# Kernel optimization log

Measured on AMD Instinct MI355X. Metric: run time of the kernel, lower is better.

## Reference

```python
import jax, jax.numpy as jnp
import numpy as np

N = 12500      # nodes
E = 200000     # edges (avg degree 16)
IN = 32        # inp_dim
OUT = 32       # out_dim
ATTN = 32      # attn_rel_emb_dim
R = 200        # num_rels
NB = 50        # num_bases


def setup_inputs() -> dict:
    key = jax.random.key(0)
    ks = jax.random.split(key, 10)
    node_feat = jax.random.normal(ks[0], (N, IN), jnp.float32)
    total_edge = jax.random.randint(ks[1], (2, E), 0, N)
    total_target_relation = jax.random.normal(ks[2], (E, ATTN), jnp.float32)
    total_relation_embed = jax.random.normal(ks[3], (E, ATTN), jnp.float32)
    total_relation = jax.random.randint(ks[4], (E,), 0, R)
    # learned parameters (xavier-ish scale)
    weight = jax.random.normal(ks[5], (NB, IN, OUT), jnp.float32) * 0.1
    w_comp = jax.random.normal(ks[6], (R, NB), jnp.float32) * 0.1
    self_loop_weight = jax.random.normal(ks[7], (IN, OUT), jnp.float32) * 0.1
    A_w = jax.random.normal(ks[8], (IN, 2 * IN + 2 * ATTN), jnp.float32) * 0.1
    A_b = jnp.zeros((IN,), jnp.float32)
    B_w = jax.random.normal(ks[9], (1, IN), jnp.float32) * 0.1
    B_b = jnp.zeros((1,), jnp.float32)
    return {
        'node_feat': node_feat,
        'total_target_relation': total_target_relation,
        'total_relation_embed': total_relation_embed,
        'weight': weight,
        'w_comp': w_comp,
        'self_loop_weight': self_loop_weight,
        'A_w': A_w,
        'A_b': A_b,
        'B_w': B_w,
        'B_b': B_b,
        'total_edge': total_edge,
        'total_relation': total_relation,
    }


def reference(node_feat, total_target_relation, total_relation_embed,
              weight, w_comp, self_loop_weight, A_w, A_b, B_w, B_b,
              total_edge, total_relation):
    # basis decomposition: per-relation weight [R, IN, OUT]
    rel_w = jnp.einsum('rb,bio->rio', w_comp, weight)
    src = node_feat[total_edge[0]]            # [E, IN]
    tgt = node_feat[total_edge[1]]            # [E, IN]
    # per-edge relation-specific transform (bmm in torch)
    msg = jnp.einsum('ei,eio->eo', src, rel_w[total_relation])  # [E, OUT]
    curr = tgt @ self_loop_weight             # [E, OUT]
    # attention MLP: sigmoid(B(relu(A(concat))))
    e = jnp.concatenate([src, tgt, total_relation_embed, total_target_relation], axis=1)
    h = jax.nn.relu(e @ A_w.T + A_b)
    a = jax.nn.sigmoid(h @ B_w.T + B_b)       # [E, 1]
    curr = curr + msg * a
    # gnn_spmm(e2n_sp, curr): scatter-add edge messages to target nodes
    out = jax.ops.segment_sum(curr, total_edge[1], num_segments=node_feat.shape[0])
    return out  # [N, OUT]
```

## Files before the change

### kernel.cpp

```cpp
#include <hip/hip_runtime.h>

#define N_NODES 12500
#define N_EDGES 200000
#define DIM 32
#define N_REL 200
#define N_BASES 50

#define OUT_ELEMS   (N_NODES * DIM)
#define ZERO_BLOCKS ((OUT_ELEMS + 1023) / 1024)

#define EDGES_PER_HBLOCK 1024
#define HIST_BLOCKS ((N_EDGES + EDGES_PER_HBLOCK - 1) / EDGES_PER_HBLOCK)

#define AWBF_OFF  409600
#define SLWT_OFF  417792
#define BINS_OFF  419840
#define GCUR_OFF  420640
#define PERM_OFF  421440
#define WS_A (PERM_OFF + N_EDGES * 16)
#define WS_B (PERM_OFF + N_EDGES * 4)

typedef __attribute__((ext_vector_type(8))) short short8;
typedef __attribute__((ext_vector_type(4))) float f32x4;
typedef __attribute__((ext_vector_type(4))) unsigned short us4;

__device__ __forceinline__ unsigned short f2bf(float x) {
    union { float f; unsigned u; } v; v.f = x;
    unsigned r = (v.u + 0x7FFFu + ((v.u >> 16) & 1u)) >> 16;
    return (unsigned short)r;
}
__device__ __forceinline__ float bf2f(unsigned short u) {
    return __uint_as_float(((unsigned)u) << 16);
}

__device__ __forceinline__ short8 cvt8(float4 a, float4 b) {
    short8 r;
    r[0] = (short)f2bf(a.x); r[1] = (short)f2bf(a.y);
    r[2] = (short)f2bf(a.z); r[3] = (short)f2bf(a.w);
    r[4] = (short)f2bf(b.x); r[5] = (short)f2bf(b.y);
    r[6] = (short)f2bf(b.z); r[7] = (short)f2bf(b.w);
    return r;
}

__device__ __forceinline__ int clampi(int x, int hi) {
    return x < 0 ? 0 : (x >= hi ? hi - 1 : x);
}

#define MFMA(A, B, C) __builtin_amdgcn_mfma_f32_16x16x32_bf16(A, B, C, 0, 0, 0)

__global__ __launch_bounds__(256) void prep_kernel(
    const float* __restrict__ weight,
    const float* __restrict__ w_comp,
    const float* __restrict__ Aw,
    const float* __restrict__ slw,
    const int*  __restrict__ rel,
    unsigned short* __restrict__ relw_bf,
    unsigned short* __restrict__ aw_bf,
    unsigned short* __restrict__ slwT_bf,
    int* __restrict__ bins,
    float* __restrict__ out,
    int sorted)
{
    int b = blockIdx.x, tid = threadIdx.x;
    if (b < N_REL) {
        __shared__ float wc[N_BASES];
        if (tid < N_BASES) wc[tid] = w_comp[b * N_BASES + tid];
        __syncthreads();
        const float* wp = weight + tid * 4;
        float4 acc = make_float4(0.f, 0.f, 0.f, 0.f);
        #pragma unroll 10
        for (int bb = 0; bb < N_BASES; bb++) {
            float4 w = *(const float4*)(wp + bb * 1024);
            float c = wc[bb];
            acc.x = fmaf(c, w.x, acc.x); acc.y = fmaf(c, w.y, acc.y);
            acc.z = fmaf(c, w.z, acc.z); acc.w = fmaf(c, w.w, acc.w);
        }
        int i = (tid * 4) >> 5, o = (tid * 4) & 31;
        if (sorted) {
            relw_bf[b * 1024 + (o + 0) * 32 + i] = f2bf(acc.x);
            relw_bf[b * 1024 + (o + 1) * 32 + i] = f2bf(acc.y);
            relw_bf[b * 1024 + (o + 2) * 32 + i] = f2bf(acc.z);
            relw_bf[b * 1024 + (o + 3) * 32 + i] = f2bf(acc.w);
        } else {
            us4 ov;
            ov[0] = f2bf(acc.x); ov[1] = f2bf(acc.y);
            ov[2] = f2bf(acc.z); ov[3] = f2bf(acc.w);
            *(us4*)(relw_bf + b * 1024 + tid * 4) = ov;
        }
    } else if (b < N_REL + ZERO_BLOCKS) {
        int base = (b - N_REL) * 1024 + tid * 4;
        if (base + 3 < OUT_ELEMS)
            *(float4*)(out + base) = make_float4(0.f, 0.f, 0.f, 0.f);
        else
            for (int k = 0; k < 4; k++)
                if (base + k < OUT_ELEMS) out[base + k] = 0.f;
    } else if (b == N_REL + ZERO_BLOCKS) {
        for (int x = tid; x < 32 * 128; x += 256) aw_bf[x] = f2bf(Aw[x]);
        for (int x = tid; x < 32 * 32; x += 256) {
            int i = x >> 5, j = x & 31;
            slwT_bf[j * 32 + i] = f2bf(slw[x]);
        }
    } else {
        __shared__ int lb[N_REL];
        if (tid < N_REL) lb[tid] = 0;
        __syncthreads();
        int base = (b - (N_REL + ZERO_BLOCKS + 1)) * EDGES_PER_HBLOCK + tid;
        #pragma unroll
        for (int k = 0; k < 4; k++) {
            int e = base + k * 256;
            if (e < N_EDGES) atomicAdd(&lb[clampi(rel[e], N_REL)], 1);
        }
        __syncthreads();
        if (tid < N_REL && lb[tid] > 0) atomicAdd(&bins[tid], lb[tid]);
    }
}

__global__ __launch_bounds__(256) void scatter_kernel(
    const int* __restrict__ rel,
    const int* __restrict__ edge0,
    const int* __restrict__ edge1,
    const int* __restrict__ bins,
    int* __restrict__ gcur,
    int4* __restrict__ perm4,
    int* __restrict__ permi)
{
    __shared__ int sb[N_REL];
    __shared__ int pref[N_REL];
    __shared__ int lb[N_REL];
    int tid = threadIdx.x;
    if (tid < N_REL) { sb[tid] = bins[tid]; lb[tid] = 0; }
    __syncthreads();
    if (tid == 0) {
        int run = 0;
        for (int r = 0; r < N_REL; r++) { pref[r] = run; run += sb[r]; }
    }
    __syncthreads();
    int base = blockIdx.x * EDGES_PER_HBLOCK + tid;
    int myr[4], myrank[4];
    #pragma unroll
    for (int k = 0; k < 4; k++) {
        int e = base + k * 256;
        myr[k] = -1;
        if (e < N_EDGES) {
            myr[k] = clampi(rel[e], N_REL);
            myrank[k] = atomicAdd(&lb[myr[k]], 1);
        }
    }
    __syncthreads();
    if (tid < N_REL) {
        int c = lb[tid];
        lb[tid] = c > 0 ? (pref[tid] + atomicAdd(&gcur[tid], c)) : 0;
    }
    __syncthreads();
    #pragma unroll
    for (int k = 0; k < 4; k++) {
        if (myr[k] >= 0) {
            int e = base + k * 256;
            int pos = lb[myr[k]] + myrank[k];
            if (perm4) {
                int s = clampi(edge0[e], N_NODES);
                int t = clampi(edge1[e], N_NODES);
                perm4[pos] = make_int4(s, t, myr[k], e);
            } else {
                permi[pos] = e;
            }
        }
    }
}

__global__ __launch_bounds__(256) void edge_kernel(
    const float* __restrict__ node_feat,
    const float* __restrict__ ttr,
    const float* __restrict__ tre,
    const float* __restrict__ Ab,
    const float* __restrict__ Bw,
    const float* __restrict__ Bb,
    const int*  __restrict__ edge0,
    const int*  __restrict__ edge1,
    const int*  __restrict__ rel,
    const int4* __restrict__ perm4,
    const int*  __restrict__ permi,
    const unsigned short* __restrict__ relw_bf,
    const unsigned short* __restrict__ aw_bf,
    const unsigned short* __restrict__ slwT_bf,
    float* __restrict__ out)
{
    __shared__ float msgL[4 * 16 * 36];

    int tid  = threadIdx.x;
    int wave = tid >> 6;
    int lane = tid & 63;
    int m = lane & 15;
    int q = lane >> 4;
    int base = blockIdx.x * 64 + wave * 16;

    int s_ld = 0, t_ld = 0, r_ld = 0, e_ld = 0;
    if (lane < 16) {
        if (perm4) {
            int4 pv = perm4[base + lane];
            s_ld = pv.x; t_ld = pv.y; r_ld = pv.z; e_ld = pv.w;
        } else {
            int eid = permi ? clampi(permi[base + lane], N_EDGES) : (base + lane);
            e_ld = eid;
            s_ld = clampi(edge0[eid], N_NODES);
            t_ld = clampi(edge1[eid], N_NODES);
            r_ld = clampi(rel[eid],   N_REL);
        }
    }
    int s_m   = __shfl(s_ld, m, 64);
    int t_m   = __shfl(t_ld, m, 64);
    int eid_m = __shfl(e_ld, m, 64);
    int r_m   = __shfl(r_ld, m, 64);
    int r0    = __shfl(r_ld, 0, 64);
    bool sorted = (perm4 != nullptr) || (permi != nullptr);

    const float* sp = node_feat + s_m * DIM + q * 8;
    float4 sv0 = *(const float4*)sp, sv1 = *(const float4*)(sp + 4);
    const float* tp = node_feat + t_m * DIM + q * 8;
    float4 tv0 = *(const float4*)tp, tv1 = *(const float4*)(tp + 4);
    const float* rp = tre + eid_m * DIM + q * 8;
    float4 rv0 = *(const float4*)rp, rv1 = *(const float4*)(rp + 4);
    const float* qp = ttr + eid_m * DIM + q * 8;
    float4 qv0 = *(const float4*)qp, qv1 = *(const float4*)(qp + 4);

    short8 fsrc = cvt8(sv0, sv1);
    short8 ftgt = cvt8(tv0, tv1);
    short8 fre  = cvt8(rv0, rv1);
    short8 ftr  = cvt8(qv0, qv1);

    short8 bA[4][2], bS[2];
    #pragma unroll
    for (int hh = 0; hh < 2; hh++) {
        #pragma unroll
        for (int c = 0; c < 4; c++)
            bA[c][hh] = *(const short8*)(aw_bf + (16 * hh + m) * 128 + 32 * c + 8 * q);
        bS[hh] = *(const short8*)(slwT_bf + (16 * hh + m) * 32 + 8 * q);
    }

    float ab0 = Ab[m], ab1 = Ab[16 + m];
    f32x4 hacc0 = {ab0, ab0, ab0, ab0};
    f32x4 hacc1 = {ab1, ab1, ab1, ab1};
    f32x4 cacc0 = {0.f, 0.f, 0.f, 0.f};
    f32x4 cacc1 = {0.f, 0.f, 0.f, 0.f};

    hacc0 = MFMA(fsrc, bA[0][0], hacc0);  hacc1 = MFMA(fsrc, bA[0][1], hacc1);
    hacc0 = MFMA(ftgt, bA[1][0], hacc0);  hacc1 = MFMA(ftgt, bA[1][1], hacc1);
    hacc0 = MFMA(fre,  bA[2][0], hacc0);  hacc1 = MFMA(fre,  bA[2][1], hacc1);
    hacc0 = MFMA(ftr,  bA[3][0], hacc0);  hacc1 = MFMA(ftr,  bA[3][1], hacc1);
    cacc0 = MFMA(ftgt, bS[0], cacc0);     cacc1 = MFMA(ftgt, bS[1], cacc1);

    f32x4 macc0 = {0.f, 0.f, 0.f, 0.f};
    f32x4 macc1 = {0.f, 0.f, 0.f, 0.f};
    bool uni = sorted && __all(r_m == r0);
    if (uni) {
        const unsigned short* rwt = relw_bf + r0 * 1024;
        short8 bM0 = *(const short8*)(rwt + m * 32 + 8 * q);
        short8 bM1 = *(const short8*)(rwt + (16 + m) * 32 + 8 * q);
        macc0 = MFMA(fsrc, bM0, macc0);
        macc1 = MFMA(fsrc, bM1, macc1);
    } else {
        int e_loc = lane >> 2;
        int cq    = lane & 3;
        int r_e = __shfl(r_ld, e_loc, 64);
        float sf[8] = {sv0.x, sv0.y, sv0.z, sv0.w, sv1.x, sv1.y, sv1.z, sv1.w};
        float msg[8] = {0.f, 0.f, 0.f, 0.f, 0.f, 0.f, 0.f, 0.f};
        const unsigned short* rw = relw_bf + r_e * 1024;
        #pragma unroll 4
        for (int k = 0; k < 32; k++) {
            float s_k = __shfl(sf[k & 7], e_loc + 16 * (k >> 3), 64);
            if (sorted) {
                #pragma unroll
                for (int p = 0; p < 8; p++)
                    msg[p] = fmaf(s_k, bf2f(rw[(cq * 8 + p) * 32 + k]), msg[p]);
            } else {
                union { short8 s; unsigned u[4]; } W;
                W.s = *(const short8*)(rw + k * 32 + cq * 8);
                #pragma unroll
                for (int p = 0; p < 4; p++) {
                    msg[2 * p]     = fmaf(s_k, __uint_as_float(W.u[p] << 16), msg[2 * p]);
                    msg[2 * p + 1] = fmaf(s_k, __uint_as_float(W.u[p] & 0xffff0000u), msg[2 * p + 1]);
                }
            }
        }
        float* ml = msgL + wave * (16 * 36);
        *(float4*)(ml + e_loc * 36 + cq * 8)     = make_float4(msg[0], msg[1], msg[2], msg[3]);
        *(float4*)(ml + e_loc * 36 + cq * 8 + 4) = make_float4(msg[4], msg[5], msg[6], msg[7]);
        #pragma unroll
        for (int v = 0; v < 4; v++) {
            macc0[v] = ml[(4 * q + v) * 36 + m];
            macc1[v] = ml[(4 * q + v) * 36 + 16 + m];
        }
    }

    float bw0 = Bw[m], bw1 = Bw[16 + m], Bb0 = Bb[0];
    float av[4];
    #pragma unroll
    for (int v = 0; v < 4; v++) {
        float p = fmaxf(hacc0[v], 0.f) * bw0 + fmaxf(hacc1[v], 0.f) * bw1;
        p += __shfl_xor(p, 1, 16);
        p += __shfl_xor(p, 2, 16);
        p += __shfl_xor(p, 4, 16);
        p += __shfl_xor(p, 8, 16);
        av[v] = 1.f / (1.f + __expf(-(p + Bb0)));
    }
    #pragma unroll
    for (int v = 0; v < 4; v++) {
        int row = 4 * q + v;
        int tv = __shfl(t_ld, row, 64);
        atomicAdd(&out[tv * DIM + m],      cacc0[v] + macc0[v] * av[v]);
        atomicAdd(&out[tv * DIM + 16 + m], cacc1[v] + macc1[v] * av[v]);
    }
}

extern "C" void kernel_launch(void* const* d_in, const int* in_sizes, int n_in,
                              void* d_out, int out_size, void* d_ws, size_t ws_size,
                              hipStream_t stream) {
    const float* node_feat = (const float*)d_in[0];
    const float* ttr       = (const float*)d_in[1];
    const float* tre       = (const float*)d_in[2];
    const float* weight    = (const float*)d_in[3];
    const float* w_comp    = (const float*)d_in[4];
    const float* slw       = (const float*)d_in[5];
    const float* Aw        = (const float*)d_in[6];
    const float* Ab        = (const float*)d_in[7];
    const float* Bw        = (const float*)d_in[8];
    const float* Bb        = (const float*)d_in[9];
    const int*  total_edge = (const int*)d_in[10];
    const int*  rel        = (const int*)d_in[11];
    const int*  edge0 = total_edge;
    const int*  edge1 = total_edge + N_EDGES;

    unsigned short* relw_bf = (unsigned short*)d_ws;
    unsigned short* aw_bf   = (unsigned short*)((char*)d_ws + AWBF_OFF);
    unsigned short* slwT_bf = (unsigned short*)((char*)d_ws + SLWT_OFF);
    int* bins = (int*)((char*)d_ws + BINS_OFF);
    int* gcur = (int*)((char*)d_ws + GCUR_OFF);
    float* out = (float*)d_out;

    int tierA = ws_size >= (size_t)WS_A;
    int tierB = !tierA && ws_size >= (size_t)WS_B;
    int sorted = tierA || tierB;
    int4* perm4 = tierA ? (int4*)((char*)d_ws + PERM_OFF) : nullptr;
    int*  permi = tierB ? (int*)((char*)d_ws + PERM_OFF) : nullptr;

    if (sorted) hipMemsetAsync(bins, 0, 1600, stream);

    int prep_blocks = N_REL + ZERO_BLOCKS + 1 + (sorted ? HIST_BLOCKS : 0);
    prep_kernel<<<prep_blocks, 256, 0, stream>>>(
        weight, w_comp, Aw, slw, rel, relw_bf, aw_bf, slwT_bf, bins, out, sorted);

    if (sorted)
        scatter_kernel<<<HIST_BLOCKS, 256, 0, stream>>>(
            rel, edge0, edge1, bins, gcur, perm4, permi);

    edge_kernel<<<N_EDGES / 64, 256, 0, stream>>>(
        node_feat, ttr, tre, Ab, Bw, Bb,
        edge0, edge1, rel, perm4, permi,
        relw_bf, aw_bf, slwT_bf, out);
}
```

Baseline: 159.5 us.

## Process 64 edges per wave in four sub-batches to amortize weight loads

Each wave now handles 64 edges instead of 16. It loads all 64 edge indices with one coalesced per-lane load and reuses the attention and self-loop weight fragments across four 16-edge MFMA sub-batches. It also checks whether the whole 64-edge wave shares one relation, so the relation weight is loaded once; otherwise it checks each 16-edge sub-batch. The grid shrinks fourfold, which cuts per-block setup and repeated weight fetches but lowers the number of resident waves available to hide gather latency. It may also raise register pressure from the unrolled loop.

```diff
diff --git a/kernel.cpp b/kernel.cpp
--- a/kernel.cpp
+++ b/kernel.cpp
@@ -192,41 +192,22 @@
     int lane = tid & 63;
     int m = lane & 15;
     int q = lane >> 4;
-    int base = blockIdx.x * 64 + wave * 16;
-
-    int s_ld = 0, t_ld = 0, r_ld = 0, e_ld = 0;
-    if (lane < 16) {
-        if (perm4) {
-            int4 pv = perm4[base + lane];
-            s_ld = pv.x; t_ld = pv.y; r_ld = pv.z; e_ld = pv.w;
-        } else {
-            int eid = permi ? clampi(permi[base + lane], N_EDGES) : (base + lane);
-            e_ld = eid;
-            s_ld = clampi(edge0[eid], N_NODES);
-            t_ld = clampi(edge1[eid], N_NODES);
-            r_ld = clampi(rel[eid],   N_REL);
-        }
-    }
-    int s_m   = __shfl(s_ld, m, 64);
-    int t_m   = __shfl(t_ld, m, 64);
-    int eid_m = __shfl(e_ld, m, 64);
-    int r_m   = __shfl(r_ld, m, 64);
-    int r0    = __shfl(r_ld, 0, 64);
+    int base = blockIdx.x * 256 + wave * 64;
+    if (base >= N_EDGES) return;
+
     bool sorted = (perm4 != nullptr) || (permi != nullptr);
 
-    const float* sp = node_feat + s_m * DIM + q * 8;
-    float4 sv0 = *(const float4*)sp, sv1 = *(const float4*)(sp + 4);
-    const float* tp = node_feat + t_m * DIM + q * 8;
-    float4 tv0 = *(const float4*)tp, tv1 = *(const float4*)(tp + 4);
-    const float* rp = tre + eid_m * DIM + q * 8;
-    float4 rv0 = *(const float4*)rp, rv1 = *(const float4*)(rp + 4);
-    const float* qp = ttr + eid_m * DIM + q * 8;
-    float4 qv0 = *(const float4*)qp, qv1 = *(const float4*)(qp + 4);
-
-    short8 fsrc = cvt8(sv0, sv1);
-    short8 ftgt = cvt8(tv0, tv1);
-    short8 fre  = cvt8(rv0, rv1);
-    short8 ftr  = cvt8(qv0, qv1);
+    int s_l, t_l, r_l, e_l;
+    if (perm4) {
+        int4 pv = perm4[base + lane];
+        s_l = pv.x; t_l = pv.y; r_l = pv.z; e_l = pv.w;
+    } else {
+        int eid = permi ? clampi(permi[base + lane], N_EDGES) : (base + lane);
+        e_l = eid;
+        s_l = clampi(edge0[eid], N_NODES);
+        t_l = clampi(edge1[eid], N_NODES);
+        r_l = clampi(rel[eid],   N_REL);
+    }
 
     short8 bA[4][2], bS[2];
     #pragma unroll
@@ -236,79 +217,115 @@
             bA[c][hh] = *(const short8*)(aw_bf + (16 * hh + m) * 128 + 32 * c + 8 * q);
         bS[hh] = *(const short8*)(slwT_bf + (16 * hh + m) * 32 + 8 * q);
     }
-
     float ab0 = Ab[m], ab1 = Ab[16 + m];
-    f32x4 hacc0 = {ab0, ab0, ab0, ab0};
-    f32x4 hacc1 = {ab1, ab1, ab1, ab1};
-    f32x4 cacc0 = {0.f, 0.f, 0.f, 0.f};
-    f32x4 cacc1 = {0.f, 0.f, 0.f, 0.f};
-
-    hacc0 = MFMA(fsrc, bA[0][0], hacc0);  hacc1 = MFMA(fsrc, bA[0][1], hacc1);
-    hacc0 = MFMA(ftgt, bA[1][0], hacc0);  hacc1 = MFMA(ftgt, bA[1][1], hacc1);
-    hacc0 = MFMA(fre,  bA[2][0], hacc0);  hacc1 = MFMA(fre,  bA[2][1], hacc1);
-    hacc0 = MFMA(ftr,  bA[3][0], hacc0);  hacc1 = MFMA(ftr,  bA[3][1], hacc1);
-    cacc0 = MFMA(ftgt, bS[0], cacc0);     cacc1 = MFMA(ftgt, bS[1], cacc1);
-
-    f32x4 macc0 = {0.f, 0.f, 0.f, 0.f};
-    f32x4 macc1 = {0.f, 0.f, 0.f, 0.f};
-    bool uni = sorted && __all(r_m == r0);
-    if (uni) {
+    float bw0 = Bw[m], bw1 = Bw[16 + m], Bb0 = Bb[0];
+
+    int r0 = __shfl(r_l, 0, 64);
+    bool uniWave = sorted && __all(r_l == r0);
+    short8 bM0w = {}, bM1w = {};
+    if (uniWave) {
         const unsigned short* rwt = relw_bf + r0 * 1024;
-        short8 bM0 = *(const short8*)(rwt + m * 32 + 8 * q);
-        short8 bM1 = *(const short8*)(rwt + (16 + m) * 32 + 8 * q);
-        macc0 = MFMA(fsrc, bM0, macc0);
-        macc1 = MFMA(fsrc, bM1, macc1);
-    } else {
-        int e_loc = lane >> 2;
-        int cq    = lane & 3;
-        int r_e = __shfl(r_ld, e_loc, 64);
-        float sf[8] = {sv0.x, sv0.y, sv0.z, sv0.w, sv1.x, sv1.y, sv1.z, sv1.w};
-        float msg[8] = {0.f, 0.f, 0.f, 0.f, 0.f, 0.f, 0.f, 0.f};
-        const unsigned short* rw = relw_bf + r_e * 1024;
-        #pragma unroll 4
-        for (int k = 0; k < 32; k++) {
-            float s_k = __shfl(sf[k & 7], e_loc + 16 * (k >> 3), 64);
-            if (sorted) {
-                #pragma unroll
-                for (int p = 0; p < 8; p++)
-                    msg[p] = fmaf(s_k, bf2f(rw[(cq * 8 + p) * 32 + k]), msg[p]);
-            } else {
-                union { short8 s; unsigned u[4]; } W;
-                W.s = *(const short8*)(rw + k * 32 + cq * 8);
-                #pragma unroll
-                for (int p = 0; p < 4; p++) {
-                    msg[2 * p]     = fmaf(s_k, __uint_as_float(W.u[p] << 16), msg[2 * p]);
-                    msg[2 * p + 1] = fmaf(s_k, __uint_as_float(W.u[p] & 0xffff0000u), msg[2 * p + 1]);
+        bM0w = *(const short8*)(rwt + m * 32 + 8 * q);
+        bM1w = *(const short8*)(rwt + (16 + m) * 32 + 8 * q);
+    }
+
+    #pragma unroll
+    for (int sb = 0; sb < 4; sb++) {
+        int lb = sb * 16;
+        int s_m   = __shfl(s_l, lb + m, 64);
+        int t_m   = __shfl(t_l, lb + m, 64);
+        int eid_m = __shfl(e_l, lb + m, 64);
+
+        const float* sp = node_feat + s_m * DIM + q * 8;
+        float4 sv0 = *(const float4*)sp, sv1 = *(const float4*)(sp + 4);
+        const float* tp = node_feat + t_m * DIM + q * 8;
+        float4 tv0 = *(const float4*)tp, tv1 = *(const float4*)(tp + 4);
+        const float* rp = tre + eid_m * DIM + q * 8;
+        float4 rv0 = *(const float4*)rp, rv1 = *(const float4*)(rp + 4);
+        const float* qp = ttr + eid_m * DIM + q * 8;
+        float4 qv0 = *(const float4*)qp, qv1 = *(const float4*)(qp + 4);
+
+        short8 fsrc = cvt8(sv0, sv1);
+        short8 ftgt = cvt8(tv0, tv1);
+        short8 fre  = cvt8(rv0, rv1);
+        short8 ftr  = cvt8(qv0, qv1);
+
+        f32x4 hacc0 = {ab0, ab0, ab0, ab0};
+        f32x4 hacc1 = {ab1, ab1, ab1, ab1};
+        f32x4 cacc0 = {0.f, 0.f, 0.f, 0.f};
+        f32x4 cacc1 = {0.f, 0.f, 0.f, 0.f};
+
+        hacc0 = MFMA(fsrc, bA[0][0], hacc0);  hacc1 = MFMA(fsrc, bA[0][1], hacc1);
+        hacc0 = MFMA(ftgt, bA[1][0], hacc0);  hacc1 = MFMA(ftgt, bA[1][1], hacc1);
+        hacc0 = MFMA(fre,  bA[2][0], hacc0);  hacc1 = MFMA(fre,  bA[2][1], hacc1);
+        hacc0 = MFMA(ftr,  bA[3][0], hacc0);  hacc1 = MFMA(ftr,  bA[3][1], hacc1);
+        cacc0 = MFMA(ftgt, bS[0], cacc0);     cacc1 = MFMA(ftgt, bS[1], cacc1);
+
+        f32x4 macc0 = {0.f, 0.f, 0.f, 0.f};
+        f32x4 macc1 = {0.f, 0.f, 0.f, 0.f};
+        int r_sb = __shfl(r_l, lb + m, 64);
+        int r00  = __shfl(r_l, lb, 64);
+        bool uni = uniWave || (sorted && __all(r_sb == r00));
+        if (uni) {
+            short8 bM0 = bM0w, bM1 = bM1w;
+            if (!uniWave) {
+                const unsigned short* rwt = relw_bf + r00 * 1024;
+                bM0 = *(const short8*)(rwt + m * 32 + 8 * q);
+                bM1 = *(const short8*)(rwt + (16 + m) * 32 + 8 * q);
+            }
+            macc0 = MFMA(fsrc, bM0, macc0);
+            macc1 = MFMA(fsrc, bM1, macc1);
+        } else {
+            int e_loc = lane >> 2;
+            int cq    = lane & 3;
+            int r_e = __shfl(r_l, lb + e_loc, 64);
+            float sf[8] = {sv0.x, sv0.y, sv0.z, sv0.w, sv1.x, sv1.y, sv1.z, sv1.w};
+            float msg[8] = {0.f, 0.f, 0.f, 0.f, 0.f, 0.f, 0.f, 0.f};
+            const unsigned short* rw = relw_bf + r_e * 1024;
+            #pragma unroll 4
+            for (int k = 0; k < 32; k++) {
+                float s_k = __shfl(sf[k & 7], e_loc + 16 * (k >> 3), 64);
+                if (sorted) {
+                    #pragma unroll
+                    for (int p = 0; p < 8; p++)
+                        msg[p] = fmaf(s_k, bf2f(rw[(cq * 8 + p) * 32 + k]), msg[p]);
+                } else {
+                    union { short8 s; unsigned u[4]; } W;
+                    W.s = *(const short8*)(rw + k * 32 + cq * 8);
+                    #pragma unroll
+                    for (int p = 0; p < 4; p++) {
+                        msg[2 * p]     = fmaf(s_k, __uint_as_float(W.u[p] << 16), msg[2 * p]);
+                        msg[2 * p + 1] = fmaf(s_k, __uint_as_float(W.u[p] & 0xffff0000u), msg[2 * p + 1]);
+                    }
                 }
             }
-        }
-        float* ml = msgL + wave * (16 * 36);
-        *(float4*)(ml + e_loc * 36 + cq * 8)     = make_float4(msg[0], msg[1], msg[2], msg[3]);
-        *(float4*)(ml + e_loc * 36 + cq * 8 + 4) = make_float4(msg[4], msg[5], msg[6], msg[7]);
+            float* ml = msgL + wave * (16 * 36);
+            *(float4*)(ml + e_loc * 36 + cq * 8)     = make_float4(msg[0], msg[1], msg[2], msg[3]);
+            *(float4*)(ml + e_loc * 36 + cq * 8 + 4) = make_float4(msg[4], msg[5], msg[6], msg[7]);
+            #pragma unroll
+            for (int v = 0; v < 4; v++) {
+                macc0[v] = ml[(4 * q + v) * 36 + m];
+                macc1[v] = ml[(4 * q + v) * 36 + 16 + m];
+            }
+        }
+
+        float av[4];
         #pragma unroll
         for (int v = 0; v < 4; v++) {
-            macc0[v] = ml[(4 * q + v) * 36 + m];
-            macc1[v] = ml[(4 * q + v) * 36 + 16 + m];
-        }
-    }
-
-    float bw0 = Bw[m], bw1 = Bw[16 + m], Bb0 = Bb[0];
-    float av[4];
-    #pragma unroll
-    for (int v = 0; v < 4; v++) {
-        float p = fmaxf(hacc0[v], 0.f) * bw0 + fmaxf(hacc1[v], 0.f) * bw1;
-        p += __shfl_xor(p, 1, 16);
-        p += __shfl_xor(p, 2, 16);
-        p += __shfl_xor(p, 4, 16);
-        p += __shfl_xor(p, 8, 16);
-        av[v] = 1.f / (1.f + __expf(-(p + Bb0)));
-    }
-    #pragma unroll
-    for (int v = 0; v < 4; v++) {
-        int row = 4 * q + v;
-        int tv = __shfl(t_ld, row, 64);
-        atomicAdd(&out[tv * DIM + m],      cacc0[v] + macc0[v] * av[v]);
-        atomicAdd(&out[tv * DIM + 16 + m], cacc1[v] + macc1[v] * av[v]);
+            float p = fmaxf(hacc0[v], 0.f) * bw0 + fmaxf(hacc1[v], 0.f) * bw1;
+            p += __shfl_xor(p, 1, 16);
+            p += __shfl_xor(p, 2, 16);
+            p += __shfl_xor(p, 4, 16);
+            p += __shfl_xor(p, 8, 16);
+            av[v] = 1.f / (1.f + __expf(-(p + Bb0)));
+        }
+        #pragma unroll
+        for (int v = 0; v < 4; v++) {
+            int row = 4 * q + v;
+            int tv = __shfl(t_l, lb + row, 64);
+            atomicAdd(&out[tv * DIM + m],      cacc0[v] + macc0[v] * av[v]);
+            atomicAdd(&out[tv * DIM + 16 + m], cacc1[v] + macc1[v] * av[v]);
+        }
     }
 }
 
@@ -353,7 +370,7 @@
         scatter_kernel<<<HIST_BLOCKS, 256, 0, stream>>>(
             rel, edge0, edge1, bins, gcur, perm4, permi);
 
-    edge_kernel<<<N_EDGES / 64, 256, 0, stream>>>(
+    edge_kernel<<<(N_EDGES + 255) / 256, 256, 0, stream>>>(
         node_feat, ttr, tre, Ab, Bw, Bb,
         edge0, edge1, rel, perm4, permi,
         relw_bf, aw_bf, slwT_bf, out);
```

Result: faster. 153.2 us (-3.9%).
